# Kernel optimization log

Measured on AMD Instinct MI355X. Metric: run time of the kernel, lower is better.

The kernel has to match this reference:

```python
import jax, jax.numpy as jnp
import numpy as np

N = 50000          # nodes
E = 1600000        # edges (avg degree 32)
B = 64             # graphs in batch
D_NODE = 128
D_EDGE = 64
D_EMB = 128
D_HID = 2 * D_EMB  # GCN output channels
EPS = 1e-5


def setup_inputs() -> dict:
    key = jax.random.key(0)
    ks = jax.random.split(key, 12)
    g = lambda k, shape: jax.random.normal(k, shape, jnp.float32) * (shape[0] ** -0.5)
    return {
        "x": jax.random.normal(ks[0], (N, D_NODE), jnp.float32),
        "edge_attr": jax.random.normal(ks[1], (E, D_EDGE), jnp.float32),
        "edge_index": jax.random.randint(ks[2], (2, E), 0, N),
        "batch": jnp.sort(jax.random.randint(ks[3], (N,), 0, B)),
        # GCNConv params
        "W1": g(ks[4], (D_NODE, D_HID)), "b1": jnp.zeros((D_HID,), jnp.float32),
        # TransformerConv params (heads=1)
        "Wq": g(ks[5], (D_HID, D_EMB)), "bq": jnp.zeros((D_EMB,), jnp.float32),
        "Wk": g(ks[6], (D_HID, D_EMB)), "bk": jnp.zeros((D_EMB,), jnp.float32),
        "Wv": g(ks[7], (D_HID, D_EMB)), "bv": jnp.zeros((D_EMB,), jnp.float32),
        "We": g(ks[8], (D_EDGE, D_EMB)), "be": jnp.zeros((D_EMB,), jnp.float32),
        "Wr": g(ks[9], (D_HID, D_EMB)), "br": jnp.zeros((D_EMB,), jnp.float32),
        # LayerNorm params
        "gamma": jnp.ones((D_EMB,), jnp.float32), "beta": jnp.zeros((D_EMB,), jnp.float32),
    }


def _forward(x, edge_attr, edge_index, batch,
             W1, b1, Wq, bq, Wk, bk, Wv, bv, We, be, Wr, br, gamma, beta):
    src, dst = edge_index[0], edge_index[1]

    # ---- GCNConv: symmetric normalization with self-loops ----
    xw = x @ W1                                                # [N, D_HID]
    deg = 1.0 + jax.ops.segment_sum(jnp.ones((E,), x.dtype), dst, num_segments=N)
    dinv = jax.lax.rsqrt(deg)                                  # deg >= 1
    norm = dinv[src] * dinv[dst]                               # [E]
    agg = jax.ops.segment_sum(xw[src] * norm[:, None], dst, num_segments=N)
    h = agg + xw * (dinv * dinv)[:, None] + b1                 # self-loop term
    h = jax.nn.relu(h)                                         # dropout = identity (eval)

    # ---- TransformerConv (heads=1, edge_dim) ----
    q = h @ Wq + bq                                            # [N, D_EMB]
    k = h @ Wk + bk
    v = h @ Wv + bv
    e = edge_attr @ We + be                                    # [E, D_EMB]
    k_j = k[src] + e
    v_j = v[src] + e
    logits = jnp.sum(q[dst] * k_j, axis=-1) / jnp.sqrt(jnp.float32(D_EMB))  # [E]
    # segment softmax over incoming edges of each target node
    lmax = jax.ops.segment_max(logits, dst, num_segments=N)
    exp_l = jnp.exp(logits - lmax[dst])
    denom = jax.ops.segment_sum(exp_l, dst, num_segments=N)
    alpha = exp_l / denom[dst]                                 # [E]
    out = jax.ops.segment_sum(alpha[:, None] * v_j, dst, num_segments=N)
    out = out + h @ Wr + br                                    # root/skip connection

    # ---- LayerNorm + ReLU ----
    mu = jnp.mean(out, axis=-1, keepdims=True)
    var = jnp.var(out, axis=-1, keepdims=True)
    out = (out - mu) * jax.lax.rsqrt(var + EPS) * gamma + beta
    out = jax.nn.relu(out)

    # ---- global mean pool over graphs ----
    sums = jax.ops.segment_sum(out, batch, num_segments=B)     # [B, D_EMB]
    cnts = jax.ops.segment_sum(jnp.ones((N,), out.dtype), batch, num_segments=B)
    return sums / jnp.maximum(cnts, 1.0)[:, None]


def reference(x, edge_attr, edge_index, batch,
              W1, b1, Wq, bq, Wk, bk, Wv, bv, We, be, Wr, br, gamma, beta):
    return _forward(x, edge_attr, edge_index, batch,
                    W1, b1, Wq, bq, Wk, bk, Wv, bv, We, be, Wr, br, gamma, beta)
```

## Files before the change

kernel.cpp:

```cpp
#include <hip/hip_runtime.h>

typedef short bf16x8 __attribute__((ext_vector_type(8)));
typedef float f32x4 __attribute__((ext_vector_type(4)));

#define DN 128
#define DE 64
#define DEMB 128
#define DHID 256
#define SCALE 0.08838834764831845f

__device__ __forceinline__ ushort f2bf(float f) {
  unsigned u = __float_as_uint(f);
  return (ushort)((u + 0x7FFFu + ((u >> 16) & 1u)) >> 16);
}
__device__ __forceinline__ float bf2f(ushort u) {
  return __uint_as_float((unsigned)u << 16);
}

__global__ void k_prep_all(const float* __restrict__ W1, const float* __restrict__ Wq,
                           const float* __restrict__ Wk, const float* __restrict__ Wv,
                           const float* __restrict__ Wr, const float* __restrict__ We,
                           const float* __restrict__ bq, const float* __restrict__ bk,
                           const float* __restrict__ bv, const float* __restrict__ br,
                           const float* __restrict__ be,
                           ushort* __restrict__ Wp1, ushort* __restrict__ Wp2,
                           ushort* __restrict__ Wp3, float* __restrict__ bcat) {
  int bid = blockIdx.x;
  if (bid < 576) {
    int idx = bid * 256 + threadIdx.x;
    int j = idx & 7, lane = (idx >> 3) & 63, s = (idx >> 9) & 7, t = idx >> 12;
    int k = s * 32 + (lane >> 4) * 8 + j;
    int c = t * 16 + (lane & 15);
    float v;
    if (c < 128)       v = Wq[k * DEMB + c] * SCALE;
    else if (c < 256)  v = Wk[k * DEMB + (c - 128)];
    else if (c < 384)  v = Wv[k * DEMB + (c - 256)];
    else if (c < 512)  v = Wr[k * DEMB + (c - 384)];
    else {
      int cc = c - 512;
      float a = 0.f;
      for (int u = 0; u < DEMB; ++u) a += Wq[k * DEMB + u] * We[cc * DEMB + u];
      v = a * SCALE;
    }
    Wp2[idx] = f2bf(v);
  } else if (bid < 704) {
    int idx = (bid - 576) * 256 + threadIdx.x;
    int j = idx & 7, lane = (idx >> 3) & 63, s = (idx >> 9) & 3, t = idx >> 11;
    int k = s * 32 + (lane >> 4) * 8 + j;
    int c = t * 16 + (lane & 15);
    Wp1[idx] = f2bf(W1[k * DHID + c]);
  } else if (bid < 736) {
    int idx = (bid - 704) * 256 + threadIdx.x;
    int j = idx & 7, lane = (idx >> 3) & 63, s = (idx >> 9) & 1, t = idx >> 10;
    int k = s * 32 + (lane >> 4) * 8 + j;
    int c = t * 16 + (lane & 15);
    Wp3[idx] = f2bf(We[k * DEMB + c]);
  } else {
    int j = (bid - 736) * 256 + threadIdx.x;
    if (j >= 576) return;
    float v;
    if (j < 128)       v = bq[j] * SCALE;
    else if (j < 256)  v = bk[j - 128] + be[j - 128];
    else if (j < 384)  v = bv[j - 256] + be[j - 256];
    else if (j < 512)  v = br[j - 384];
    else {
      int cc = j - 512;
      float a = 0.f;
      for (int u = 0; u < DEMB; ++u) a += bq[u] * We[cc * DEMB + u];
      v = a * SCALE;
    }
    bcat[j] = v;
  }
}

__global__ void k_deg(const int* __restrict__ ei, int* __restrict__ degi, int nE) {
  int e = blockIdx.x * 256 + threadIdx.x;
  if (e < nE) atomicAdd(&degi[ei[nE + e]], 1);
}

__global__ __launch_bounds__(1024) void k_scan(const int* __restrict__ degi,
                                               int* __restrict__ row_ptr,
                                               float* __restrict__ dinv, int n) {
  __shared__ int wsum[16];
  __shared__ int carry_s;
  int lane = threadIdx.x & 63, wid = threadIdx.x >> 6;
  if (threadIdx.x == 0) carry_s = 0;
  __syncthreads();
  for (int base = 0; base < n; base += 1024) {
    int i = base + threadIdx.x;
    int v = (i < n) ? degi[i] : 0;
    if (i < n) dinv[i] = rsqrtf(1.0f + (float)v);
    int sc = v;
    #pragma unroll
    for (int off = 1; off < 64; off <<= 1) {
      int t = __shfl_up(sc, off);
      if (lane >= off) sc += t;
    }
    if (lane == 63) wsum[wid] = sc;
    int carry0 = carry_s;
    __syncthreads();
    if (wid == 0) {
      int w = (lane < 16) ? wsum[lane] : 0;
      int swc = w;
      #pragma unroll
      for (int off = 1; off < 16; off <<= 1) {
        int t = __shfl_up(swc, off);
        if (lane >= off) swc += t;
      }
      if (lane < 16) wsum[lane] = swc - w;
      if (lane == 15) carry_s = carry0 + swc;
    }
    __syncthreads();
    if (i < n) row_ptr[i] = carry0 + wsum[wid] + sc - v;
    __syncthreads();
  }
  if (threadIdx.x == 0) row_ptr[n] = carry_s;
}

__global__ void k_scatter(const int* __restrict__ ei, const int* __restrict__ row_ptr,
                          int* __restrict__ cursor, int2* __restrict__ csr_se, int nE) {
  int e = blockIdx.x * 256 + threadIdx.x;
  if (e >= nE) return;
  int dst = ei[nE + e];
  int pos = row_ptr[dst] + atomicAdd(&cursor[dst], 1);
  csr_se[pos] = make_int2(ei[e], e);
}

__global__ __launch_bounds__(256) void k_xcast(const float* __restrict__ x,
                                               const float* __restrict__ dinv,
                                               const int* __restrict__ batch,
                                               int* __restrict__ gstart,
                                               ushort* __restrict__ xsb, int nN, int B) {
  int idx = blockIdx.x * 256 + threadIdx.x;
  if (idx < nN) {
    int b = batch[idx];
    if (idx == 0) {
      for (int g = 0; g <= b; ++g) gstart[g] = 0;
    } else {
      int pb = batch[idx - 1];
      for (int g = pb + 1; g <= b; ++g) gstart[g] = idx;
    }
    if (idx == nN - 1) {
      for (int g = b + 1; g <= B; ++g) gstart[g] = nN;
    }
  }
  if (idx < nN * 32) {
    int n = idx >> 5, q = idx & 31;
    float dn = dinv[n];
    float4 v = *(const float4*)&x[(size_t)n * DN + q * 4];
    ushort4 o;
    o.x = f2bf(v.x * dn); o.y = f2bf(v.y * dn);
    o.z = f2bf(v.z * dn); o.w = f2bf(v.w * dn);
    *(ushort4*)&xsb[(size_t)n * DN + q * 4] = o;
  }
}

__global__ __launch_bounds__(256) void k_gcnX(const ushort* __restrict__ xsb,
                                              const int2* __restrict__ csr_se,
                                              const int* __restrict__ row_ptr,
                                              const float* __restrict__ dinv,
                                              ushort* __restrict__ aggxb, int nN) {
  int lane = threadIdx.x & 63;
  int n = blockIdx.x * 4 + (threadIdx.x >> 6);
  if (n >= nN) return;
  int grp = lane >> 4, l15 = lane & 15;
  int beg = row_ptr[n], end = row_ptr[n + 1];
  float acc[8] = {};
  for (int i0 = beg; i0 < end; i0 += 32) {
    int src[8]; bool vl[8];
    #pragma unroll
    for (int u = 0; u < 8; ++u) {
      int e = i0 + u * 4 + grp;
      vl[u] = e < end;
      src[u] = csr_se[vl[u] ? e : end - 1].x;
    }
    uint4 xa[8];
    #pragma unroll
    for (int u = 0; u < 8; ++u)
      xa[u] = *(const uint4*)&xsb[(size_t)src[u] * DN + l15 * 8];
    #pragma unroll
    for (int u = 0; u < 8; ++u) {
      float w = vl[u] ? 1.f : 0.f;
      unsigned qq[4] = {xa[u].x, xa[u].y, xa[u].z, xa[u].w};
      #pragma unroll
      for (int d = 0; d < 4; ++d) {
        acc[2*d]   = fmaf(w, __uint_as_float(qq[d] << 16), acc[2*d]);
        acc[2*d+1] = fmaf(w, __uint_as_float(qq[d] & 0xFFFF0000u), acc[2*d+1]);
      }
    }
  }
  #pragma unroll
  for (int d = 0; d < 8; ++d) {
    acc[d] += __shfl_xor(acc[d], 16);
    acc[d] += __shfl_xor(acc[d], 32);
  }
  if (grp == 0) {
    uint4 sa = *(const uint4*)&xsb[(size_t)n * DN + l15 * 8];
    unsigned sq[4] = {sa.x, sa.y, sa.z, sa.w};
    float dn = dinv[n];
    ushort o[8];
    #pragma unroll
    for (int d = 0; d < 4; ++d) {
      float lo = __uint_as_float(sq[d] << 16);
      float hi = __uint_as_float(sq[d] & 0xFFFF0000u);
      o[2*d]   = f2bf(dn * (acc[2*d]   + lo));
      o[2*d+1] = f2bf(dn * (acc[2*d+1] + hi));
    }
    uint4 ov = {(unsigned)o[0] | ((unsigned)o[1] << 16),
                (unsigned)o[2] | ((unsigned)o[3] << 16),
                (unsigned)o[4] | ((unsigned)o[5] << 16),
                (unsigned)o[6] | ((unsigned)o[7] << 16)};
    *(uint4*)&aggxb[(size_t)n * DN + l15 * 8] = ov;
  }
}

__global__ __launch_bounds__(256) void k_gemm1b(const ushort* __restrict__ aggxb,
                                                const ushort* __restrict__ Wp1,
                                                const float* __restrict__ b1,
                                                ushort* __restrict__ hb, int nN) {
  int lane = threadIdx.x & 63, wave = threadIdx.x >> 6;
  int l15 = lane & 15, lh = lane >> 4;
  int m0 = blockIdx.x * 16;
  int rowa = m0 + l15; if (rowa >= nN) rowa = nN - 1;
  f32x4 acc[4] = {};
  #pragma unroll
  for (int s = 0; s < 4; ++s) {
    bf16x8 af = *(const bf16x8*)&aggxb[(size_t)rowa * DN + s * 32 + lh * 8];
    #pragma unroll
    for (int tt = 0; tt < 4; ++tt) {
      int t = wave * 4 + tt;
      bf16x8 bf = *(const bf16x8*)&Wp1[((t * 4 + s) * 64 + lane) * 8];
      acc[tt] = __builtin_amdgcn_mfma_f32_16x16x32_bf16(af, bf, acc[tt], 0, 0, 0);
    }
  }
  #pragma unroll
  for (int tt = 0; tt < 4; ++tt) {
    int c = (wave * 4 + tt) * 16 + l15;
    float bc = b1[c];
    #pragma unroll
    for (int r = 0; r < 4; ++r) {
      int row = m0 + lh * 4 + r;
      if (row < nN) hb[(size_t)row * DHID + c] = f2bf(fmaxf(acc[tt][r] + bc, 0.f));
    }
  }
}

__global__ __launch_bounds__(256) void k_gemm2(const ushort* __restrict__ hb,
                                               const ushort* __restrict__ Wp2,
                                               const float* __restrict__ bcat,
                                               ushort* __restrict__ qwb,
                                               ushort* __restrict__ kb,
                                               ushort* __restrict__ vb,
                                               ushort* __restrict__ hrb, int nN) {
  int lane = threadIdx.x & 63, wave = threadIdx.x >> 6;
  int l15 = lane & 15, lh = lane >> 4;
  int m0 = blockIdx.x * 16;
  int rowa = m0 + l15; if (rowa >= nN) rowa = nN - 1;
  f32x4 acc[9] = {};
  for (int s = 0; s < 8; ++s) {
    bf16x8 af = *(const bf16x8*)&hb[(size_t)rowa * DHID + s * 32 + lh * 8];
    #pragma unroll
    for (int tt = 0; tt < 9; ++tt) {
      int t = wave * 9 + tt;
      bf16x8 bf = *(const bf16x8*)&Wp2[((t * 8 + s) * 64 + lane) * 8];
      acc[tt] = __builtin_amdgcn_mfma_f32_16x16x32_bf16(af, bf, acc[tt], 0, 0, 0);
    }
  }
  #pragma unroll
  for (int tt = 0; tt < 9; ++tt) {
    int c = (wave * 9 + tt) * 16 + l15;
    float bc = bcat[c];
    #pragma unroll
    for (int r = 0; r < 4; ++r) {
      int row = m0 + lh * 4 + r;
      if (row >= nN) continue;
      ushort val = f2bf(acc[tt][r] + bc);
      if (c < 128)      qwb[(size_t)row * 192 + c] = val;
      else if (c < 256) kb[(size_t)row * 128 + (c - 128)] = val;
      else if (c < 384) vb[(size_t)row * 128 + (c - 256)] = val;
      else if (c < 512) hrb[(size_t)row * 128 + (c - 384)] = val;
      else              qwb[(size_t)row * 192 + 128 + (c - 512)] = val;
    }
  }
}

__global__ __launch_bounds__(256, 4) void k_edge(const ushort* __restrict__ qwb,
                                                 const ushort* __restrict__ kb,
                                                 const ushort* __restrict__ vb,
                                                 const float* __restrict__ ea32,
                                                 const int2* __restrict__ csr_se,
                                                 const int* __restrict__ row_ptr,
                                                 float* __restrict__ sden,
                                                 float* __restrict__ vaccf,
                                                 ushort* __restrict__ ewb, int nN) {
  int lane = threadIdx.x & 63;
  int n = blockIdx.x * 4 + (threadIdx.x >> 6);
  if (n >= nN) return;
  int grp = lane >> 4, l15 = lane & 15;
  const ushort* qp = &qwb[(size_t)n * 192];
  bf16x8 qv = *(const bf16x8*)&qp[l15 * 8];
  ushort4 wv = *(const ushort4*)&qp[128 + l15 * 4];
  float q[8];
  #pragma unroll
  for (int d = 0; d < 8; ++d) q[d] = bf2f((ushort)qv[d]);
  float w0 = bf2f(wv.x), w1 = bf2f(wv.y), w2 = bf2f(wv.z), w3 = bf2f(wv.w);
  float s_acc = 0.f;
  float av[8] = {};
  float ae[4] = {};
  int beg = row_ptr[n], end = row_ptr[n + 1];
  for (int i0 = beg; i0 < end; i0 += 24) {
    int2 se[6]; bool vl[6];
    #pragma unroll
    for (int u = 0; u < 6; ++u) {
      int e = i0 + u * 4 + grp;
      vl[u] = e < end;
      se[u] = csr_se[vl[u] ? e : end - 1];
    }
    bf16x8 kv8[6]; bf16x8 vv8[6]; float4 eav[6];
    #pragma unroll
    for (int u = 0; u < 6; ++u) {
      kv8[u] = *(const bf16x8*)&kb[(size_t)se[u].x * 128 + l15 * 8];
      vv8[u] = *(const bf16x8*)&vb[(size_t)se[u].x * 128 + l15 * 8];
      eav[u] = *(const float4*)&ea32[(size_t)se[u].y * DE + l15 * 4];
    }
    #pragma unroll
    for (int u = 0; u < 6; ++u) {
      float dot = w0 * eav[u].x + w1 * eav[u].y + w2 * eav[u].z + w3 * eav[u].w;
      #pragma unroll
      for (int d = 0; d < 8; ++d) dot = fmaf(q[d], bf2f((ushort)kv8[u][d]), dot);
      dot += __shfl_xor(dot, 1);
      dot += __shfl_xor(dot, 2);
      dot += __shfl_xor(dot, 4);
      dot += __shfl_xor(dot, 8);
      float p = vl[u] ? __expf(dot) : 0.f;
      s_acc += p;
      #pragma unroll
      for (int d = 0; d < 8; ++d) av[d] = fmaf(p, bf2f((ushort)vv8[u][d]), av[d]);
      ae[0] = fmaf(p, eav[u].x, ae[0]);
      ae[1] = fmaf(p, eav[u].y, ae[1]);
      ae[2] = fmaf(p, eav[u].z, ae[2]);
      ae[3] = fmaf(p, eav[u].w, ae[3]);
    }
  }
  s_acc += __shfl_xor(s_acc, 16); s_acc += __shfl_xor(s_acc, 32);
  #pragma unroll
  for (int d = 0; d < 8; ++d) {
    av[d] += __shfl_xor(av[d], 16);
    av[d] += __shfl_xor(av[d], 32);
  }
  #pragma unroll
  for (int d = 0; d < 4; ++d) {
    ae[d] += __shfl_xor(ae[d], 16);
    ae[d] += __shfl_xor(ae[d], 32);
  }
  if (grp == 0) {
    if (l15 == 0) sden[n] = s_acc;
    float4 o0 = {av[0], av[1], av[2], av[3]};
    float4 o1 = {av[4], av[5], av[6], av[7]};
    float* vr = &vaccf[(size_t)n * 128 + l15 * 8];
    *(float4*)vr = o0;
    *(float4*)(vr + 4) = o1;
    ushort4 eo;
    eo.x = f2bf(ae[0]); eo.y = f2bf(ae[1]); eo.z = f2bf(ae[2]); eo.w = f2bf(ae[3]);
    *(ushort4*)&ewb[(size_t)n * DE + l15 * 4] = eo;
  }
}

__global__ __launch_bounds__(256) void k_ewe(const ushort* __restrict__ ewb,
                                             const ushort* __restrict__ Wp3,
                                             float* __restrict__ ewout, int nN) {
  int lane = threadIdx.x & 63, wave = threadIdx.x >> 6;
  int l15 = lane & 15, lh = lane >> 4;
  int m0 = blockIdx.x * 16;
  int rowa = m0 + l15; if (rowa >= nN) rowa = nN - 1;
  f32x4 acc[2] = {};
  #pragma unroll
  for (int s = 0; s < 2; ++s) {
    bf16x8 af = *(const bf16x8*)&ewb[(size_t)rowa * DE + s * 32 + lh * 8];
    #pragma unroll
    for (int tt = 0; tt < 2; ++tt) {
      int t = wave * 2 + tt;
      bf16x8 bf = *(const bf16x8*)&Wp3[((t * 2 + s) * 64 + lane) * 8];
      acc[tt] = __builtin_amdgcn_mfma_f32_16x16x32_bf16(af, bf, acc[tt], 0, 0, 0);
    }
  }
  #pragma unroll
  for (int tt = 0; tt < 2; ++tt) {
    int c = (wave * 2 + tt) * 16 + l15;
    #pragma unroll
    for (int r = 0; r < 4; ++r) {
      int row = m0 + lh * 4 + r;
      if (row < nN) ewout[(size_t)row * 128 + c] = acc[tt][r];
    }
  }
}

__global__ __launch_bounds__(256) void k_fin(const float* __restrict__ sden,
                                             const float* __restrict__ vaccf,
                                             const float* __restrict__ ewout,
                                             const ushort* __restrict__ hrb,
                                             const float* __restrict__ gamma,
                                             const float* __restrict__ beta,
                                             float* __restrict__ ynorm, int nN) {
  int lane = threadIdx.x & 63, grp = lane >> 5, l5 = lane & 31;
  int n = blockIdx.x * 8 + (threadIdx.x >> 6) * 2 + grp;
  if (n >= nN) return;
  float s = sden[n];
  float inv = (s > 0.f) ? 1.f / s : 0.f;
  float4 v4 = *(const float4*)&vaccf[(size_t)n * 128 + l5 * 4];
  float4 w4 = *(const float4*)&ewout[(size_t)n * 128 + l5 * 4];
  ushort4 hv = *(const ushort4*)&hrb[(size_t)n * 128 + l5 * 4];
  float4 o4;
  o4.x = (v4.x + w4.x) * inv + bf2f(hv.x);
  o4.y = (v4.y + w4.y) * inv + bf2f(hv.y);
  o4.z = (v4.z + w4.z) * inv + bf2f(hv.z);
  o4.w = (v4.w + w4.w) * inv + bf2f(hv.w);
  float s1 = o4.x + o4.y + o4.z + o4.w;
  float sq = o4.x*o4.x + o4.y*o4.y + o4.z*o4.z + o4.w*o4.w;
  #pragma unroll
  for (int off = 1; off < 32; off <<= 1) {
    s1 += __shfl_xor(s1, off);
    sq += __shfl_xor(sq, off);
  }
  float mu = s1 * (1.f / 128.f);
  float var = sq * (1.f / 128.f) - mu * mu;
  float rstd = rsqrtf(var + 1e-5f);
  float4 g4 = *(const float4*)&gamma[l5 * 4];
  float4 b4 = *(const float4*)&beta[l5 * 4];
  float4 y;
  y.x = fmaxf((o4.x - mu) * rstd * g4.x + b4.x, 0.f);
  y.y = fmaxf((o4.y - mu) * rstd * g4.y + b4.y, 0.f);
  y.z = fmaxf((o4.z - mu) * rstd * g4.z + b4.z, 0.f);
  y.w = fmaxf((o4.w - mu) * rstd * g4.w + b4.w, 0.f);
  *(float4*)&ynorm[(size_t)n * 128 + l5 * 4] = y;
}

__global__ __launch_bounds__(128) void k_pool(const float* __restrict__ ynorm,
                                              const int* __restrict__ gstart,
                                              float* __restrict__ out) {
  int b = blockIdx.x, t = threadIdx.x;
  int beg = gstart[b], end = gstart[b + 1];
  float a0 = 0.f, a1 = 0.f, a2 = 0.f, a3 = 0.f;
  int n = beg;
  for (; n + 4 <= end; n += 4) {
    a0 += ynorm[(size_t)(n + 0) * 128 + t];
    a1 += ynorm[(size_t)(n + 1) * 128 + t];
    a2 += ynorm[(size_t)(n + 2) * 128 + t];
    a3 += ynorm[(size_t)(n + 3) * 128 + t];
  }
  for (; n < end; ++n) a0 += ynorm[(size_t)n * 128 + t];
  float acc = (a0 + a1) + (a2 + a3);
  out[b * 128 + t] = acc / fmaxf((float)(end - beg), 1.f);
}

extern "C" void kernel_launch(void* const* d_in, const int* in_sizes, int n_in,
                              void* d_out, int out_size, void* d_ws, size_t ws_size,
                              hipStream_t stream) {
  const float* x         = (const float*)d_in[0];
  const float* edge_attr = (const float*)d_in[1];
  const int*   edge_index= (const int*)d_in[2];
  const int*   batch     = (const int*)d_in[3];
  const float* W1 = (const float*)d_in[4];
  const float* b1 = (const float*)d_in[5];
  const float* Wq = (const float*)d_in[6];  const float* bq = (const float*)d_in[7];
  const float* Wk = (const float*)d_in[8];  const float* bk = (const float*)d_in[9];
  const float* Wv = (const float*)d_in[10]; const float* bv = (const float*)d_in[11];
  const float* We = (const float*)d_in[12]; const float* be = (const float*)d_in[13];
  const float* Wr = (const float*)d_in[14]; const float* br = (const float*)d_in[15];
  const float* gamma = (const float*)d_in[16];
  const float* beta  = (const float*)d_in[17];
  float* out = (float*)d_out;

  const int nN = in_sizes[0] / DN;
  const int nE = in_sizes[1] / DE;
  const int B  = out_size / DEMB;

  char* p = (char*)d_ws;
  auto alloc = [&](size_t bytes) -> void* {
    void* r = (void*)p;
    p += (bytes + 255) & ~(size_t)255;
    return r;
  };
  int*   degi   = (int*)  alloc((size_t)nN * 4);
  int*   cursor = (int*)  alloc((size_t)nN * 4);
  size_t zero_bytes = (size_t)(p - (char*)d_ws);
  int*    row_ptr = (int*)   alloc((size_t)(nN + 1) * 4);
  int*    gstart  = (int*)   alloc((size_t)(B + 1) * 4);
  float*  dinv    = (float*) alloc((size_t)nN * 4);
  int2*   csr_se  = (int2*)  alloc((size_t)nE * 8);
  ushort* Wp1     = (ushort*)alloc((size_t)16 * 4 * 64 * 8 * 2);
  ushort* Wp2     = (ushort*)alloc((size_t)36 * 8 * 64 * 8 * 2);
  ushort* Wp3     = (ushort*)alloc((size_t)8 * 2 * 64 * 8 * 2);
  float*  bcat    = (float*) alloc(576 * 4);
  ushort* qwb     = (ushort*)alloc((size_t)nN * 192 * 2);
  ushort* hrb     = (ushort*)alloc((size_t)nN * 128 * 2);
  ushort* hb      = (ushort*)alloc((size_t)nN * DHID * 2);
  ushort* xsb     = (ushort*)alloc((size_t)nN * DN * 2);
  ushort* aggxb   = (ushort*)alloc((size_t)nN * DN * 2);
  ushort* kb      = xsb;
  ushort* vb      = aggxb;
  float*  sden    = (float*) alloc((size_t)nN * 4);
  float*  vaccf   = (float*) alloc((size_t)nN * 128 * 4);
  ushort* ewb     = (ushort*)alloc((size_t)nN * DE * 2);
  float*  ewout   = (float*) alloc((size_t)nN * 128 * 4);
  float*  ynorm   = (float*) alloc((size_t)nN * 128 * 4);
  size_t required = (size_t)(p - (char*)d_ws);
  if (ws_size < required) return;

  hipMemsetAsync(d_ws, 0, zero_bytes, stream);

  k_prep_all<<<739, 256, 0, stream>>>(W1, Wq, Wk, Wv, Wr, We, bq, bk, bv, br, be,
                                      Wp1, Wp2, Wp3, bcat);
  k_deg<<<(nE + 255) / 256, 256, 0, stream>>>(edge_index, degi, nE);
  k_scan<<<1, 1024, 0, stream>>>(degi, row_ptr, dinv, nN);
  k_scatter<<<(nE + 255) / 256, 256, 0, stream>>>(edge_index, row_ptr, cursor,
                                                  csr_se, nE);
  k_xcast<<<(nN * 32 + 255) / 256, 256, 0, stream>>>(x, dinv, batch, gstart, xsb,
                                                     nN, B);
  k_gcnX<<<(nN + 3) / 4, 256, 0, stream>>>(xsb, csr_se, row_ptr, dinv, aggxb, nN);
  k_gemm1b<<<(nN + 15) / 16, 256, 0, stream>>>(aggxb, Wp1, b1, hb, nN);
  k_gemm2<<<(nN + 15) / 16, 256, 0, stream>>>(hb, Wp2, bcat, qwb, kb, vb, hrb, nN);
  k_edge<<<(nN + 3) / 4, 256, 0, stream>>>(qwb, kb, vb, edge_attr, csr_se, row_ptr,
                                           sden, vaccf, ewb, nN);
  k_ewe<<<(nN + 15) / 16, 256, 0, stream>>>(ewb, Wp3, ewout, nN);
  k_fin<<<(nN + 7) / 8, 256, 0, stream>>>(sden, vaccf, ewout, hrb, gamma, beta,
                                          ynorm, nN);
  k_pool<<<B, 128, 0, stream>>>(ynorm, gstart, out);
}
```

Measured before the change: 717.8 us.

## Double-buffer gather loops in GCN and edge kernels, interleave K/V rows

Replaces the wide unrolled gather batches in k_gcnX and k_edge with a two-stage ping-pong loop. The next 8 edges' indices and feature rows are loaded while the current 8 are accumulated. K and V are written by k_gemm2 into one interleaved buffer, so each lane fetches its K and V chunks from one contiguous 32-byte span per source node. The k_edge occupancy hint is dropped. The interleaved buffer is twice the size of the xsb allocation and relies on spilling into the adjacent aggxb region. Fewer edges are in flight per iteration, which may reduce memory-level parallelism compared to the previous 24–32-edge batches.

```diff
diff --git a/kernel.cpp b/kernel.cpp
--- a/kernel.cpp
+++ b/kernel.cpp
@@ -166,29 +166,50 @@
   int grp = lane >> 4, l15 = lane & 15;
   int beg = row_ptr[n], end = row_ptr[n + 1];
   float acc[8] = {};
-  for (int i0 = beg; i0 < end; i0 += 32) {
-    int src[8]; bool vl[8];
-    #pragma unroll
-    for (int u = 0; u < 8; ++u) {
-      int e = i0 + u * 4 + grp;
-      vl[u] = e < end;
-      src[u] = csr_se[vl[u] ? e : end - 1].x;
-    }
-    uint4 xa[8];
-    #pragma unroll
-    for (int u = 0; u < 8; ++u)
-      xa[u] = *(const uint4*)&xsb[(size_t)src[u] * DN + l15 * 8];
-    #pragma unroll
-    for (int u = 0; u < 8; ++u) {
-      float w = vl[u] ? 1.f : 0.f;
-      unsigned qq[4] = {xa[u].x, xa[u].y, xa[u].z, xa[u].w};
-      #pragma unroll
-      for (int d = 0; d < 4; ++d) {
-        acc[2*d]   = fmaf(w, __uint_as_float(qq[d] << 16), acc[2*d]);
-        acc[2*d+1] = fmaf(w, __uint_as_float(qq[d] & 0xFFFF0000u), acc[2*d+1]);
-      }
-    }
-  }
+
+#define GLOAD(S0, S1, X0, X1, base)                                        \
+  {                                                                        \
+    int e0 = (base) + grp,     c0 = e0 < end ? e0 : end - 1;               \
+    int e1 = (base) + 4 + grp, c1 = e1 < end ? e1 : end - 1;               \
+    S0 = csr_se[c0].x; S1 = csr_se[c1].x;                                  \
+    X0 = *(const uint4*)&xsb[(size_t)S0 * DN + l15 * 8];                   \
+    X1 = *(const uint4*)&xsb[(size_t)S1 * DN + l15 * 8];                   \
+  }
+#define GCOMP(X0, X1, base)                                                \
+  {                                                                        \
+    float m0 = ((base) + grp < end) ? 1.f : 0.f;                           \
+    float m1 = ((base) + 4 + grp < end) ? 1.f : 0.f;                       \
+    unsigned q0[4] = {X0.x, X0.y, X0.z, X0.w};                             \
+    unsigned q1[4] = {X1.x, X1.y, X1.z, X1.w};                             \
+    _Pragma("unroll") for (int d = 0; d < 4; ++d) {                        \
+      acc[2*d]   = fmaf(m0, __uint_as_float(q0[d] << 16), acc[2*d]);       \
+      acc[2*d+1] = fmaf(m0, __uint_as_float(q0[d] & 0xFFFF0000u), acc[2*d+1]); \
+      acc[2*d]   = fmaf(m1, __uint_as_float(q1[d] << 16), acc[2*d]);       \
+      acc[2*d+1] = fmaf(m1, __uint_as_float(q1[d] & 0xFFFF0000u), acc[2*d+1]); \
+    }                                                                      \
+  }
+
+  if (beg < end) {
+    int sA0, sA1, sB0, sB1;
+    uint4 xA0, xA1, xB0, xB1;
+    int i0 = beg;
+    GLOAD(sA0, sA1, xA0, xA1, i0);
+    while (true) {
+      int i1 = i0 + 8;
+      if (i1 < end) GLOAD(sB0, sB1, xB0, xB1, i1);
+      GCOMP(xA0, xA1, i0);
+      i0 = i1;
+      if (i0 >= end) break;
+      int i2 = i0 + 8;
+      if (i2 < end) GLOAD(sA0, sA1, xA0, xA1, i2);
+      GCOMP(xB0, xB1, i0);
+      i0 = i2;
+      if (i0 >= end) break;
+    }
+  }
+#undef GLOAD
+#undef GCOMP
+
   #pragma unroll
   for (int d = 0; d < 8; ++d) {
     acc[d] += __shfl_xor(acc[d], 16);
@@ -249,8 +270,7 @@
                                                const ushort* __restrict__ Wp2,
                                                const float* __restrict__ bcat,
                                                ushort* __restrict__ qwb,
-                                               ushort* __restrict__ kb,
-                                               ushort* __restrict__ vb,
+                                               ushort* __restrict__ kvb,
                                                ushort* __restrict__ hrb, int nN) {
   int lane = threadIdx.x & 63, wave = threadIdx.x >> 6;
   int l15 = lane & 15, lh = lane >> 4;
@@ -276,23 +296,22 @@
       if (row >= nN) continue;
       ushort val = f2bf(acc[tt][r] + bc);
       if (c < 128)      qwb[(size_t)row * 192 + c] = val;
-      else if (c < 256) kb[(size_t)row * 128 + (c - 128)] = val;
-      else if (c < 384) vb[(size_t)row * 128 + (c - 256)] = val;
+      else if (c < 256) { int d = c - 128; kvb[(size_t)row * 256 + (d >> 3) * 16 + (d & 7)] = val; }
+      else if (c < 384) { int d = c - 256; kvb[(size_t)row * 256 + (d >> 3) * 16 + 8 + (d & 7)] = val; }
       else if (c < 512) hrb[(size_t)row * 128 + (c - 384)] = val;
       else              qwb[(size_t)row * 192 + 128 + (c - 512)] = val;
     }
   }
 }
 
-__global__ __launch_bounds__(256, 4) void k_edge(const ushort* __restrict__ qwb,
-                                                 const ushort* __restrict__ kb,
-                                                 const ushort* __restrict__ vb,
-                                                 const float* __restrict__ ea32,
-                                                 const int2* __restrict__ csr_se,
-                                                 const int* __restrict__ row_ptr,
-                                                 float* __restrict__ sden,
-                                                 float* __restrict__ vaccf,
-                                                 ushort* __restrict__ ewb, int nN) {
+__global__ __launch_bounds__(256) void k_edge(const ushort* __restrict__ qwb,
+                                              const ushort* __restrict__ kvb,
+                                              const float* __restrict__ ea32,
+                                              const int2* __restrict__ csr_se,
+                                              const int* __restrict__ row_ptr,
+                                              float* __restrict__ sden,
+                                              float* __restrict__ vaccf,
+                                              ushort* __restrict__ ewb, int nN) {
   int lane = threadIdx.x & 63;
   int n = blockIdx.x * 4 + (threadIdx.x >> 6);
   if (n >= nN) return;
@@ -308,40 +327,64 @@
   float av[8] = {};
   float ae[4] = {};
   int beg = row_ptr[n], end = row_ptr[n + 1];
-  for (int i0 = beg; i0 < end; i0 += 24) {
-    int2 se[6]; bool vl[6];
-    #pragma unroll
-    for (int u = 0; u < 6; ++u) {
-      int e = i0 + u * 4 + grp;
-      vl[u] = e < end;
-      se[u] = csr_se[vl[u] ? e : end - 1];
-    }
-    bf16x8 kv8[6]; bf16x8 vv8[6]; float4 eav[6];
-    #pragma unroll
-    for (int u = 0; u < 6; ++u) {
-      kv8[u] = *(const bf16x8*)&kb[(size_t)se[u].x * 128 + l15 * 8];
-      vv8[u] = *(const bf16x8*)&vb[(size_t)se[u].x * 128 + l15 * 8];
-      eav[u] = *(const float4*)&ea32[(size_t)se[u].y * DE + l15 * 4];
-    }
-    #pragma unroll
-    for (int u = 0; u < 6; ++u) {
-      float dot = w0 * eav[u].x + w1 * eav[u].y + w2 * eav[u].z + w3 * eav[u].w;
-      #pragma unroll
-      for (int d = 0; d < 8; ++d) dot = fmaf(q[d], bf2f((ushort)kv8[u][d]), dot);
-      dot += __shfl_xor(dot, 1);
-      dot += __shfl_xor(dot, 2);
-      dot += __shfl_xor(dot, 4);
-      dot += __shfl_xor(dot, 8);
-      float p = vl[u] ? __expf(dot) : 0.f;
-      s_acc += p;
-      #pragma unroll
-      for (int d = 0; d < 8; ++d) av[d] = fmaf(p, bf2f((ushort)vv8[u][d]), av[d]);
-      ae[0] = fmaf(p, eav[u].x, ae[0]);
-      ae[1] = fmaf(p, eav[u].y, ae[1]);
-      ae[2] = fmaf(p, eav[u].z, ae[2]);
-      ae[3] = fmaf(p, eav[u].w, ae[3]);
-    }
-  }
+
+#define ELOAD(SE0, SE1, K0, K1, V0, V1, E0, E1, base)                      \
+  {                                                                        \
+    int e0 = (base) + grp,     c0 = e0 < end ? e0 : end - 1;               \
+    int e1 = (base) + 4 + grp, c1 = e1 < end ? e1 : end - 1;               \
+    SE0 = csr_se[c0]; SE1 = csr_se[c1];                                    \
+    const ushort* r0 = &kvb[(size_t)SE0.x * 256 + l15 * 16];               \
+    const ushort* r1 = &kvb[(size_t)SE1.x * 256 + l15 * 16];               \
+    K0 = *(const bf16x8*)r0;  V0 = *(const bf16x8*)(r0 + 8);               \
+    K1 = *(const bf16x8*)r1;  V1 = *(const bf16x8*)(r1 + 8);               \
+    E0 = *(const float4*)&ea32[(size_t)SE0.y * DE + l15 * 4];              \
+    E1 = *(const float4*)&ea32[(size_t)SE1.y * DE + l15 * 4];              \
+  }
+#define ESLOT(K, V, E, valid)                                              \
+  {                                                                        \
+    float dot = w0 * E.x + w1 * E.y + w2 * E.z + w3 * E.w;                 \
+    _Pragma("unroll") for (int d = 0; d < 8; ++d)                          \
+      dot = fmaf(q[d], bf2f((ushort)K[d]), dot);                           \
+    dot += __shfl_xor(dot, 1);                                             \
+    dot += __shfl_xor(dot, 2);                                             \
+    dot += __shfl_xor(dot, 4);                                             \
+    dot += __shfl_xor(dot, 8);                                             \
+    float p = (valid) ? __expf(dot) : 0.f;                                 \
+    s_acc += p;                                                            \
+    _Pragma("unroll") for (int d = 0; d < 8; ++d)                          \
+      av[d] = fmaf(p, bf2f((ushort)V[d]), av[d]);                          \
+    ae[0] = fmaf(p, E.x, ae[0]); ae[1] = fmaf(p, E.y, ae[1]);              \
+    ae[2] = fmaf(p, E.z, ae[2]); ae[3] = fmaf(p, E.w, ae[3]);              \
+  }
+#define ECOMP(K0, K1, V0, V1, E0, E1, base)                                \
+  {                                                                        \
+    ESLOT(K0, V0, E0, (base) + grp < end);                                 \
+    ESLOT(K1, V1, E1, (base) + 4 + grp < end);                             \
+  }
+
+  if (beg < end) {
+    int2 seA0, seA1, seB0, seB1;
+    bf16x8 kA0, kA1, vA0, vA1, kB0, kB1, vB0, vB1;
+    float4 eA0, eA1, eB0, eB1;
+    int i0 = beg;
+    ELOAD(seA0, seA1, kA0, kA1, vA0, vA1, eA0, eA1, i0);
+    while (true) {
+      int i1 = i0 + 8;
+      if (i1 < end) ELOAD(seB0, seB1, kB0, kB1, vB0, vB1, eB0, eB1, i1);
+      ECOMP(kA0, kA1, vA0, vA1, eA0, eA1, i0);
+      i0 = i1;
+      if (i0 >= end) break;
+      int i2 = i0 + 8;
+      if (i2 < end) ELOAD(seA0, seA1, kA0, kA1, vA0, vA1, eA0, eA1, i2);
+      ECOMP(kB0, kB1, vB0, vB1, eB0, eB1, i0);
+      i0 = i2;
+      if (i0 >= end) break;
+    }
+  }
+#undef ELOAD
+#undef ESLOT
+#undef ECOMP
+
   s_acc += __shfl_xor(s_acc, 16); s_acc += __shfl_xor(s_acc, 32);
   #pragma unroll
   for (int d = 0; d < 8; ++d) {
@@ -497,8 +540,7 @@
   ushort* hb      = (ushort*)alloc((size_t)nN * DHID * 2);
   ushort* xsb     = (ushort*)alloc((size_t)nN * DN * 2);
   ushort* aggxb   = (ushort*)alloc((size_t)nN * DN * 2);
-  ushort* kb      = xsb;
-  ushort* vb      = aggxb;
+  ushort* kvb     = xsb;
   float*  sden    = (float*) alloc((size_t)nN * 4);
   float*  vaccf   = (float*) alloc((size_t)nN * 128 * 4);
   ushort* ewb     = (ushort*)alloc((size_t)nN * DE * 2);
@@ -519,8 +561,8 @@
                                                      nN, B);
   k_gcnX<<<(nN + 3) / 4, 256, 0, stream>>>(xsb, csr_se, row_ptr, dinv, aggxb, nN);
   k_gemm1b<<<(nN + 15) / 16, 256, 0, stream>>>(aggxb, Wp1, b1, hb, nN);
-  k_gemm2<<<(nN + 15) / 16, 256, 0, stream>>>(hb, Wp2, bcat, qwb, kb, vb, hrb, nN);
-  k_edge<<<(nN + 3) / 4, 256, 0, stream>>>(qwb, kb, vb, edge_attr, csr_se, row_ptr,
+  k_gemm2<<<(nN + 15) / 16, 256, 0, stream>>>(hb, Wp2, bcat, qwb, kvb, hrb, nN);
+  k_edge<<<(nN + 3) / 4, 256, 0, stream>>>(qwb, kvb, edge_attr, csr_se, row_ptr,
                                            sden, vaccf, ewb, nN);
   k_ewe<<<(nN + 15) / 16, 256, 0, stream>>>(ewb, Wp3, ewout, nN);
   k_fin<<<(nN + 7) / 8, 256, 0, stream>>>(sden, vaccf, ewout, hrb, gamma, beta,
```

New measurement: 616.8 us. -14.1%, faster.
